# Performance work log

Measured on AMD Instinct MI355X. Metric: run time of the kernel, lower is better.

The kernel has to match this reference:

```python
import math
import jax, jax.numpy as jnp
import numpy as np
from jax import lax

N = 224
EPS_BN = 1e-5


def _conv(x, w, b):
    y = lax.conv_general_dilated(x, w, (1, 1), 'SAME',
                                 dimension_numbers=('NCHW', 'OIHW', 'NCHW'))
    return y + b[None, :, None, None]


def _bn(x, g, beta, m, v):
    # eval-mode BatchNorm2d with running stats
    inv = lax.rsqrt(v + EPS_BN)
    return (x - m[None, :, None, None]) * (g * inv)[None, :, None, None] + beta[None, :, None, None]


def _maxpool2(x):
    return lax.reduce_window(x, -jnp.inf, lax.max, (1, 1, 2, 2), (1, 1, 2, 2), 'VALID')


def setup_inputs() -> dict:
    key = jax.random.key(0)
    ks = jax.random.split(key, 12)
    idx = np.arange(N, dtype=np.float32)
    angles = 2.0 * math.pi * idx[None, :] * idx[:, None] / N
    inp = {
        'sequences': jax.random.normal(ks[0], (16, 8, 3, N, N), dtype=jnp.float32),
        'dft_cos': jnp.asarray(np.cos(angles), dtype=jnp.float32),
        'dft_sin': jnp.asarray(np.sin(angles), dtype=jnp.float32),
        'conv1_w': jax.random.normal(ks[1], (16, 3, 3, 3), dtype=jnp.float32) * 0.1,
        'conv1_b': jnp.zeros((16,), jnp.float32),
        'bn1_g': jnp.ones((16,), jnp.float32),
        'bn1_b': jnp.zeros((16,), jnp.float32),
        'bn1_m': jnp.zeros((16,), jnp.float32),
        'bn1_v': jnp.ones((16,), jnp.float32),
        'conv2_w': jax.random.normal(ks[2], (32, 16, 3, 3), dtype=jnp.float32) * 0.05,
        'conv2_b': jnp.zeros((32,), jnp.float32),
        'bn2_g': jnp.ones((32,), jnp.float32),
        'bn2_b': jnp.zeros((32,), jnp.float32),
        'bn2_m': jnp.zeros((32,), jnp.float32),
        'bn2_v': jnp.ones((32,), jnp.float32),
        'conv3_w': jax.random.normal(ks[3], (64, 32, 3, 3), dtype=jnp.float32) * 0.05,
        'conv3_b': jnp.zeros((64,), jnp.float32),
        'bn3_g': jnp.ones((64,), jnp.float32),
        'bn3_b': jnp.zeros((64,), jnp.float32),
        'bn3_m': jnp.zeros((64,), jnp.float32),
        'bn3_v': jnp.ones((64,), jnp.float32),
        'fc_w': jax.random.normal(ks[4], (128, 64), dtype=jnp.float32) * 0.1,
        'fc_b': jnp.zeros((128,), jnp.float32),
    }
    return inp


def reference(sequences, dft_cos, dft_sin,
              conv1_w, conv1_b, bn1_g, bn1_b, bn1_m, bn1_v,
              conv2_w, conv2_b, bn2_g, bn2_b, bn2_m, bn2_v,
              conv3_w, conv3_b, bn3_g, bn3_b, bn3_m, bn3_v,
              fc_w, fc_b):
    b, s = sequences.shape[0], sequences.shape[1]
    x = sequences[:, s // 2]  # center frames [B,3,H,W]

    # 2D DFT via dense matmul chain: X = (C - jS) x (C - jS)
    C, S = dft_cos, dft_sin
    Cx = jnp.einsum('ij,bcjk->bcik', C, x)
    Sx = jnp.einsum('ij,bcjk->bcik', S, x)
    X_real = jnp.einsum('bcij,jk->bcik', Cx, C) - jnp.einsum('bcij,jk->bcik', Sx, S)
    X_imag = -(jnp.einsum('bcij,jk->bcik', Cx, S) + jnp.einsum('bcij,jk->bcik', Sx, C))
    magnitude = jnp.sqrt(X_real ** 2 + X_imag ** 2 + 1e-08)
    spec = jnp.log(magnitude + 1e-08)
    half = N // 2
    spec = jnp.roll(spec, shift=(half, half), axis=(-2, -1))  # fftshift

    # CNN stack (eval-mode BN, dropout disabled)
    h = jax.nn.relu(_bn(_conv(spec, conv1_w, conv1_b), bn1_g, bn1_b, bn1_m, bn1_v))
    h = _maxpool2(h)
    h = jax.nn.relu(_bn(_conv(h, conv2_w, conv2_b), bn2_g, bn2_b, bn2_m, bn2_v))
    h = _maxpool2(h)
    h = jax.nn.relu(_bn(_conv(h, conv3_w, conv3_b), bn3_g, bn3_b, bn3_m, bn3_v))
    h = jnp.mean(h, axis=(2, 3))  # AdaptiveAvgPool2d((1,1)) + flatten -> [B,64]

    freq_out = jax.nn.relu(h @ fc_w.T + fc_b)  # dropout = identity in eval
    return freq_out
```

## Files before the change

### kernel.cpp

```cpp
#include <hip/hip_runtime.h>
#include <math.h>
#include <stddef.h>

#define N224 224
#define PIX 50176
#define ROWS113 25312

#define OFF_SX    1214976
#define OFF_SPEC  4816896
#define OFF_WT    3211264
#define OFF_WT2   (OFF_WT + 24576)
#define OFF_WT1   (OFF_WT + 30720)
#define OFF_SU3   (OFF_WT + 31296)
#define OFF_SU2   (OFF_WT + 31424)
#define OFF_SU1   (OFF_WT + 31488)
#define OFF_PART  (OFF_WT + 32768)

__global__ __launch_bounds__(256) void prep(
    const float* __restrict__ c1w, const float* __restrict__ c2w,
    const float* __restrict__ c3w, const float* __restrict__ c1b,
    const float* __restrict__ c2b, const float* __restrict__ c3b,
    const float* __restrict__ g1, const float* __restrict__ be1,
    const float* __restrict__ m1, const float* __restrict__ v1,
    const float* __restrict__ g2, const float* __restrict__ be2,
    const float* __restrict__ m2, const float* __restrict__ v2,
    const float* __restrict__ g3, const float* __restrict__ be3,
    const float* __restrict__ m3, const float* __restrict__ v3,
    float* __restrict__ wt3, float* __restrict__ wt2, float* __restrict__ wt1,
    float* __restrict__ su3, float* __restrict__ su2, float* __restrict__ su1)
{
  const int idx = blockIdx.x * 256 + threadIdx.x;
  const int stride = gridDim.x * 256;
  for (int i = idx; i < 32*64*12; i += stride) {
    const int cc = i / 768, r = i % 768, co = r / 12, k = r % 12;
    wt3[i] = (k < 9) ? c3w[co*288 + cc*9 + k] : 0.f;
  }
  for (int i = idx; i < 16*32*12; i += stride) {
    const int cc = i / 384, r = i % 384, co = r / 12, k = r % 12;
    wt2[i] = (k < 9) ? c2w[co*144 + cc*9 + k] : 0.f;
  }
  for (int i = idx; i < 3*16*12; i += stride) {
    const int cc = i / 192, r = i % 192, co = r / 12, k = r % 12;
    wt1[i] = (k < 9) ? c1w[co*27 + cc*9 + k] : 0.f;
  }
  if (idx < 64) {
    const float s = g3[idx] * rsqrtf(v3[idx] + 1e-5f);
    su3[idx] = s; su3[64+idx] = (c3b[idx] - m3[idx]) * s + be3[idx];
  } else if (idx < 96) {
    const int c = idx - 64;
    const float s = g2[c] * rsqrtf(v2[c] + 1e-5f);
    su2[c] = s; su2[32+c] = (c2b[c] - m2[c]) * s + be2[c];
  } else if (idx < 112) {
    const int c = idx - 96;
    const float s = g1[c] * rsqrtf(v1[c] + 1e-5f);
    su1[c] = s; su1[16+c] = (c1b[c] - m1[c]) * s + be1[c];
  }
}

__global__ __launch_bounds__(256) void dft1(
    const float* __restrict__ seq, const float* __restrict__ Cm,
    const float* __restrict__ Sm, float* __restrict__ Cx, float* __restrict__ Sx)
{
  const int p = blockIdx.z;
  const int b = p / 3, ch = p % 3;
  const float* __restrict__ x = seq + ((((size_t)b * 8 + 4) * 3 + ch) * PIX);
  const int i0 = blockIdx.y * 32;
  const int k0 = blockIdx.x * 32;
  const int tid = threadIdx.x;
  const int tx = tid & 15, ty = tid >> 4;
  __shared__ float Ctt[16][36], Stt[16][36], Xt[16][36];
  float aC[2][2] = {{0,0},{0,0}}, aS[2][2] = {{0,0},{0,0}};

  const int sidx = tid & 127;
  const int srow = sidx >> 2;
  const int skq  = (sidx & 3) * 4;
  const bool isC = tid < 128;
  const float* __restrict__ csb = (isC ? Cm : Sm) + (size_t)(i0 + srow) * N224 + skq;
  const int xjr = tid >> 4;
  const int xc  = (tid & 15) * 2;
  const float* __restrict__ xb = x + (size_t)xjr * N224 + k0 + xc;

  for (int jt = 0; jt < 14; ++jt) {
    const int j = jt * 16;
    __syncthreads();
    {
      const float4 v = *(const float4*)(csb + j);
      float (*dst)[36] = isC ? Ctt : Stt;
      dst[skq+0][srow] = v.x; dst[skq+1][srow] = v.y;
      dst[skq+2][srow] = v.z; dst[skq+3][srow] = v.w;
      *(float2*)&Xt[xjr][xc] = *(const float2*)(xb + (size_t)j * N224);
    }
    __syncthreads();
#pragma unroll
    for (int jj = 0; jj < 16; ++jj) {
      const float2 cv = *(const float2*)&Ctt[jj][2*ty];
      const float2 sv = *(const float2*)&Stt[jj][2*ty];
      const float2 xv = *(const float2*)&Xt[jj][2*tx];
      aC[0][0] = fmaf(cv.x, xv.x, aC[0][0]); aC[0][1] = fmaf(cv.x, xv.y, aC[0][1]);
      aC[1][0] = fmaf(cv.y, xv.x, aC[1][0]); aC[1][1] = fmaf(cv.y, xv.y, aC[1][1]);
      aS[0][0] = fmaf(sv.x, xv.x, aS[0][0]); aS[0][1] = fmaf(sv.x, xv.y, aS[0][1]);
      aS[1][0] = fmaf(sv.y, xv.x, aS[1][0]); aS[1][1] = fmaf(sv.y, xv.y, aS[1][1]);
    }
  }
  const size_t b113 = (size_t)p * ROWS113;
#pragma unroll
  for (int a = 0; a < 2; ++a) {
    const int i = i0 + 2*ty + a;
    if (i <= 112) {
      const size_t off = b113 + (size_t)i * N224 + k0 + 2*tx;
      *(float2*)&Cx[off] = make_float2(aC[a][0], aC[a][1]);
      *(float2*)&Sx[off] = make_float2(aS[a][0], aS[a][1]);
    }
  }
}

__global__ __launch_bounds__(256) void dft2(
    const float* __restrict__ Cx, const float* __restrict__ Sx,
    const float* __restrict__ Cm, const float* __restrict__ Sm,
    float* __restrict__ spec)
{
  const int p = blockIdx.z;
  const int i0 = blockIdx.y * 32;
  const int k0 = blockIdx.x * 32;
  const int tid = threadIdx.x;
  const int tx = tid & 15, ty = tid >> 4;
  const size_t b113 = (size_t)p * ROWS113;
  __shared__ float CxT[16][36], SxT[16][36], Ct[16][36], St[16][36];
  float p1[2][2] = {{0,0},{0,0}}, p2[2][2] = {{0,0},{0,0}};
  float p3[2][2] = {{0,0},{0,0}}, p4[2][2] = {{0,0},{0,0}};

  const int sidx = tid & 127;
  const int srow = sidx >> 2;
  const int skq  = (sidx & 3) * 4;
  const bool isCx = tid < 128;
  const int ri = (i0 + srow > 112) ? 112 : i0 + srow;
  const float* __restrict__ ab = (isCx ? Cx : Sx) + b113 + (size_t)ri * N224 + skq;
  const int jr = tid >> 4;
  const int cc2 = (tid & 15) * 2;
  const float* __restrict__ cb = Cm + (size_t)jr * N224 + k0 + cc2;
  const float* __restrict__ sb2 = Sm + (size_t)jr * N224 + k0 + cc2;

  for (int jt = 0; jt < 14; ++jt) {
    const int j = jt * 16;
    __syncthreads();
    {
      const float4 v = *(const float4*)(ab + j);
      float (*dst)[36] = isCx ? CxT : SxT;
      dst[skq+0][srow] = v.x; dst[skq+1][srow] = v.y;
      dst[skq+2][srow] = v.z; dst[skq+3][srow] = v.w;
      *(float2*)&Ct[jr][cc2] = *(const float2*)(cb + (size_t)j * N224);
      *(float2*)&St[jr][cc2] = *(const float2*)(sb2 + (size_t)j * N224);
    }
    __syncthreads();
#pragma unroll
    for (int jj = 0; jj < 16; ++jj) {
      const float2 cxv = *(const float2*)&CxT[jj][2*ty];
      const float2 sxv = *(const float2*)&SxT[jj][2*ty];
      const float2 ccv = *(const float2*)&Ct[jj][2*tx];
      const float2 ssv = *(const float2*)&St[jj][2*tx];
      const float cxa[2] = {cxv.x, cxv.y};
      const float sxa[2] = {sxv.x, sxv.y};
      const float cca[2] = {ccv.x, ccv.y};
      const float ssa[2] = {ssv.x, ssv.y};
#pragma unroll
      for (int a = 0; a < 2; ++a)
#pragma unroll
        for (int d = 0; d < 2; ++d) {
          p1[a][d] = fmaf(cxa[a], cca[d], p1[a][d]);
          p2[a][d] = fmaf(sxa[a], ssa[d], p2[a][d]);
          p3[a][d] = fmaf(cxa[a], ssa[d], p3[a][d]);
          p4[a][d] = fmaf(sxa[a], cca[d], p4[a][d]);
        }
    }
  }
  const size_t sb = (size_t)p * PIX;
#pragma unroll
  for (int a = 0; a < 2; ++a) {
    const int i = i0 + 2*ty + a;
    if (i > 112) continue;
    const int shi  = (i < 112) ? i + 112 : i - 112;
    const int shmi = 112 - i;
    const bool irm = (i >= 1) && (i <= 111);
#pragma unroll
    for (int d = 0; d < 2; ++d) {
      const int k = k0 + 2*tx + d;
      if (k > 112) continue;
      const float r1 = p1[a][d] - p2[a][d];
      const float i1 = p3[a][d] + p4[a][d];
      const float sp1v = logf(sqrtf(fmaf(r1, r1, fmaf(i1, i1, 1e-8f))) + 1e-8f);
      const float r2v = p1[a][d] + p2[a][d];
      const float i2v = p3[a][d] - p4[a][d];
      const float sp2v = logf(sqrtf(fmaf(r2v, r2v, fmaf(i2v, i2v, 1e-8f))) + 1e-8f);
      const int shk  = (k < 112) ? k + 112 : k - 112;
      const int shmk = 112 - k;
      const bool krm = (k >= 1) && (k <= 111);
      spec[sb + (size_t)shi*N224 + shk] = sp1v;
      if (irm)        spec[sb + (size_t)shmi*N224 + shk ] = sp2v;
      if (krm)        spec[sb + (size_t)shi *N224 + shmk] = sp2v;
      if (irm && krm) spec[sb + (size_t)shmi*N224 + shmk] = sp1v;
    }
  }
}

__global__ __launch_bounds__(256) void conv1(
    const float* __restrict__ spec, const float* __restrict__ wt1,
    const float* __restrict__ su1, float* __restrict__ out)
{
  const int band = blockIdx.x, b = blockIdx.y;
  const int tid = threadIdx.x;
  const int lane = tid & 63, w = tid >> 6;
  const int co = lane & 15, cr = (lane >> 4) & 1, xs = lane >> 5;
  const int xh = w >> 1, xq = w & 1;
  __shared__ float in_t[3][4][232];
  for (int i = tid; i < 3*4*232; i += 256) {
    const int c = i % 232, r = (i / 232) % 4, cc = i / 928;
    const int y = band*2 - 1 + r, gx = c - 1;
    float v = 0.f;
    if (c < 226 && y >= 0 && y < 224 && gx >= 0 && gx < 224)
      v = spec[((size_t)b*3 + cc) * PIX + (size_t)y * N224 + gx];
    in_t[cc][r][c] = v;
  }
  __syncthreads();
  const int X0 = xh*112 + xq*56 + xs*28;
  float acc[28];
#pragma unroll
  for (int px = 0; px < 28; ++px) acc[px] = 0.f;
#pragma unroll
  for (int cc = 0; cc < 3; ++cc) {
    const float4 w0 = *(const float4*)&wt1[cc*192 + co*12];
    const float4 w1 = *(const float4*)&wt1[cc*192 + co*12 + 4];
    const float  w8 = wt1[cc*192 + co*12 + 8];
    const float wr[9] = {w0.x, w0.y, w0.z, w0.w, w1.x, w1.y, w1.z, w1.w, w8};
#pragma unroll
    for (int ky = 0; ky < 3; ++ky) {
      float xr[32];
      const float4* rp = (const float4*)&in_t[cc][cr + ky][X0];
#pragma unroll
      for (int t = 0; t < 8; ++t) {
        const float4 v = rp[t];
        xr[4*t]=v.x; xr[4*t+1]=v.y; xr[4*t+2]=v.z; xr[4*t+3]=v.w;
      }
#pragma unroll
      for (int px = 0; px < 28; ++px) {
        acc[px] = fmaf(xr[px  ], wr[ky*3  ], acc[px]);
        acc[px] = fmaf(xr[px+1], wr[ky*3+1], acc[px]);
        acc[px] = fmaf(xr[px+2], wr[ky*3+2], acc[px]);
      }
    }
  }
  const float s = su1[co], u = su1[16+co];
  float m[14];
#pragma unroll
  for (int p = 0; p < 14; ++p)
    m[p] = fmaxf(acc[2*p]*s + u, acc[2*p+1]*s + u);
#pragma unroll
  for (int p = 0; p < 14; ++p) {
    const float pm = __shfl_xor(m[p], 16);
    m[p] = fmaxf(fmaxf(m[p], pm), 0.f);
  }
  if (cr == 0) {
    const int pxb = X0 >> 1;
    float* op = &out[(((size_t)b*16 + co)*112 + band)*112 + pxb];
#pragma unroll
    for (int p = 0; p < 14; ++p) op[p] = m[p];
  }
}

__global__ __launch_bounds__(256) void conv2(
    const float* __restrict__ h1, const float* __restrict__ wt2,
    const float* __restrict__ su2, float* __restrict__ out)
{
  const int xh = blockIdx.x, band = blockIdx.y, b = blockIdx.z;
  const int tid = threadIdx.x;
  const int lane = tid & 63, w = tid >> 6;
  const int co = lane & 31, cr = lane >> 5;
  __shared__ float in_t[16][4][64];
  for (int i = tid; i < 16*4*58; i += 256) {
    const int c = i % 58, r = (i / 58) % 4, cc = i / 232;
    const int y = band*2 - 1 + r, gx = xh*56 - 1 + c;
    float v = 0.f;
    if (y >= 0 && y < 112 && gx >= 0 && gx < 112)
      v = h1[(((size_t)b*16 + cc)*112 + y)*112 + gx];
    in_t[cc][r][c] = v;
  }
  __syncthreads();
  const int X0 = w * 14;
  float acc[14];
#pragma unroll
  for (int px = 0; px < 14; ++px) acc[px] = 0.f;
  const float* __restrict__ wp = wt2 + co*12;
  float4 nw0 = *(const float4*)(wp);
  float4 nw1 = *(const float4*)(wp + 4);
  float  nw8 = wp[8];
  for (int cc = 0; cc < 16; ++cc) {
    const float4 w0 = nw0, w1 = nw1; const float w8 = nw8;
    if (cc < 15) {
      const float* np = wp + (cc + 1) * 384;
      nw0 = *(const float4*)(np);
      nw1 = *(const float4*)(np + 4);
      nw8 = np[8];
    }
    const float wr[9] = {w0.x, w0.y, w0.z, w0.w, w1.x, w1.y, w1.z, w1.w, w8};
    float xr[3][16];
#pragma unroll
    for (int ky = 0; ky < 3; ++ky) {
      const float2* rp = (const float2*)&in_t[cc][cr + ky][X0];
#pragma unroll
      for (int t = 0; t < 8; ++t) {
        const float2 v = rp[t];
        xr[ky][2*t] = v.x; xr[ky][2*t+1] = v.y;
      }
    }
#pragma unroll
    for (int ky = 0; ky < 3; ++ky)
#pragma unroll
      for (int px = 0; px < 14; ++px) {
        acc[px] = fmaf(xr[ky][px  ], wr[ky*3  ], acc[px]);
        acc[px] = fmaf(xr[ky][px+1], wr[ky*3+1], acc[px]);
        acc[px] = fmaf(xr[ky][px+2], wr[ky*3+2], acc[px]);
      }
  }
  const float s = su2[co], u = su2[32+co];
  float m[7];
#pragma unroll
  for (int p = 0; p < 7; ++p)
    m[p] = fmaxf(acc[2*p]*s + u, acc[2*p+1]*s + u);
#pragma unroll
  for (int p = 0; p < 7; ++p) {
    const float pm = __shfl_xor(m[p], 32);
    m[p] = fmaxf(fmaxf(m[p], pm), 0.f);
  }
  if (cr == 0) {
    float* op = &out[(((size_t)b*32 + co)*56 + band)*56 + xh*28 + w*7];
#pragma unroll
    for (int p = 0; p < 7; ++p) op[p] = m[p];
  }
}

__global__ __launch_bounds__(256) void conv3(
    const float* __restrict__ h2, const float* __restrict__ wt3,
    const float* __restrict__ su3, float* __restrict__ part)
{
  const int band = blockIdx.x, b = blockIdx.y;
  const int tid = threadIdx.x;
  const int co = tid & 63, w = tid >> 6;
  __shared__ float in_t[32][3][64];
  __shared__ float red[4][64];
  for (int i = tid; i < 32*3*58; i += 256) {
    const int c = i % 58, r = (i / 58) % 3, cc = i / 174;
    const int y = band - 1 + r, gx = c - 1;
    float v = 0.f;
    if (y >= 0 && y < 56 && gx >= 0 && gx < 56)
      v = h2[(((size_t)b*32 + cc)*56 + y)*56 + gx];
    in_t[cc][r][c] = v;
  }
  __syncthreads();
  const int X0 = w * 14;
  float acc[14];
#pragma unroll
  for (int px = 0; px < 14; ++px) acc[px] = 0.f;
  const float* __restrict__ wp = wt3 + co*12;
  float4 nw0 = *(const float4*)(wp);
  float4 nw1 = *(const float4*)(wp + 4);
  float  nw8 = wp[8];
  for (int cc = 0; cc < 32; ++cc) {
    const float4 w0 = nw0, w1 = nw1; const float w8 = nw8;
    if (cc < 31) {
      const float* np = wp + (cc + 1) * 768;
      nw0 = *(const float4*)(np);
      nw1 = *(const float4*)(np + 4);
      nw8 = np[8];
    }
    const float wr[9] = {w0.x, w0.y, w0.z, w0.w, w1.x, w1.y, w1.z, w1.w, w8};
    float xr[3][16];
#pragma unroll
    for (int rr = 0; rr < 3; ++rr) {
      const float2* rp = (const float2*)&in_t[cc][rr][X0];
#pragma unroll
      for (int t = 0; t < 8; ++t) {
        const float2 v = rp[t];
        xr[rr][2*t] = v.x; xr[rr][2*t+1] = v.y;
      }
    }
#pragma unroll
    for (int rr = 0; rr < 3; ++rr)
#pragma unroll
      for (int px = 0; px < 14; ++px) {
        acc[px] = fmaf(xr[rr][px  ], wr[rr*3  ], acc[px]);
        acc[px] = fmaf(xr[rr][px+1], wr[rr*3+1], acc[px]);
        acc[px] = fmaf(xr[rr][px+2], wr[rr*3+2], acc[px]);
      }
  }
  const float s = su3[co], u = su3[64+co];
  float sum = 0.f;
#pragma unroll
  for (int px = 0; px < 14; ++px)
    sum += fmaxf(acc[px]*s + u, 0.f);
  red[w][co] = sum;
  __syncthreads();
  if (tid < 64)
    part[((size_t)b*64 + co)*56 + band] =
        red[0][co] + red[1][co] + red[2][co] + red[3][co];
}

__global__ __launch_bounds__(128) void mean_fc(
    const float* __restrict__ part, const float* __restrict__ fw,
    const float* __restrict__ fb, float* __restrict__ out)
{
  const int b = blockIdx.x;
  const int tid = threadIdx.x;
  __shared__ float h3s[64];
  if (tid < 64) {
    float s = 0.f;
    const float* pp = part + ((size_t)b*64 + tid)*56;
#pragma unroll
    for (int i = 0; i < 56; ++i) s += pp[i];
    h3s[tid] = s * (1.0f / 3136.0f);
  }
  __syncthreads();
  float acc = fb[tid];
#pragma unroll
  for (int c = 0; c < 64; ++c)
    acc = fmaf(h3s[c], fw[tid*64 + c], acc);
  out[b*128 + tid] = fmaxf(acc, 0.f);
}

extern "C" void kernel_launch(void* const* d_in, const int* in_sizes, int n_in,
                              void* d_out, int out_size, void* d_ws, size_t ws_size,
                              hipStream_t stream) {
  const float* seq  = (const float*)d_in[0];
  const float* dcos = (const float*)d_in[1];
  const float* dsin = (const float*)d_in[2];
  const float* c1w  = (const float*)d_in[3];
  const float* c1b  = (const float*)d_in[4];
  const float* b1g  = (const float*)d_in[5];
  const float* b1b  = (const float*)d_in[6];
  const float* b1m  = (const float*)d_in[7];
  const float* b1v  = (const float*)d_in[8];
  const float* c2w  = (const float*)d_in[9];
  const float* c2b  = (const float*)d_in[10];
  const float* b2g  = (const float*)d_in[11];
  const float* b2b  = (const float*)d_in[12];
  const float* b2m  = (const float*)d_in[13];
  const float* b2v  = (const float*)d_in[14];
  const float* c3w  = (const float*)d_in[15];
  const float* c3b  = (const float*)d_in[16];
  const float* b3g  = (const float*)d_in[17];
  const float* b3b  = (const float*)d_in[18];
  const float* b3m  = (const float*)d_in[19];
  const float* b3v  = (const float*)d_in[20];
  const float* fw   = (const float*)d_in[21];
  const float* fb   = (const float*)d_in[22];
  float* out = (float*)d_out;

  float* ws   = (float*)d_ws;
  float* Cx   = ws;
  float* Sx   = ws + OFF_SX;
  float* spec = ws + OFF_SPEC;
  float* h1   = ws;
  float* h2   = ws + OFF_SPEC;
  float* wt3  = ws + OFF_WT;
  float* wt2  = ws + OFF_WT2;
  float* wt1  = ws + OFF_WT1;
  float* su3  = ws + OFF_SU3;
  float* su2  = ws + OFF_SU2;
  float* su1  = ws + OFF_SU1;
  float* part = ws + OFF_PART;

  prep<<<24, 256, 0, stream>>>(c1w, c2w, c3w, c1b, c2b, c3b,
                               b1g, b1b, b1m, b1v, b2g, b2b, b2m, b2v,
                               b3g, b3b, b3m, b3v, wt3, wt2, wt1, su3, su2, su1);
  dft1<<<dim3(7, 4, 48), 256, 0, stream>>>(seq, dcos, dsin, Cx, Sx);
  dft2<<<dim3(4, 4, 48), 256, 0, stream>>>(Cx, Sx, dcos, dsin, spec);
  conv1<<<dim3(112, 16), 256, 0, stream>>>(spec, wt1, su1, h1);
  conv2<<<dim3(2, 56, 16), 256, 0, stream>>>(h1, wt2, su2, h2);
  conv3<<<dim3(56, 16), 256, 0, stream>>>(h2, wt3, su3, part);
  mean_fc<<<16, 128, 0, stream>>>(part, fw, fb, out);
}
```

Measured before the change: 164.1 us.

## Register-block conv3 over two output channels with half-width pixel strips

```diff
diff --git a/kernel.cpp b/kernel.cpp
--- a/kernel.cpp
+++ b/kernel.cpp
@@ -337,14 +337,15 @@
   }
 }
 
-__global__ __launch_bounds__(256) void conv3(
+__global__ __launch_bounds__(256, 2) void conv3(
     const float* __restrict__ h2, const float* __restrict__ wt3,
     const float* __restrict__ su3, float* __restrict__ part)
 {
   const int band = blockIdx.x, b = blockIdx.y;
   const int tid = threadIdx.x;
-  const int co = tid & 63, w = tid >> 6;
-  __shared__ float in_t[32][3][64];
+  const int lane = tid & 63, w = tid >> 6;
+  const int co = lane & 31, xs = lane >> 5;
+  __shared__ float in_t[32][3][60];
   __shared__ float red[4][64];
   for (int i = tid; i < 32*3*58; i += 256) {
     const int c = i % 58, r = (i / 58) % 3, cc = i / 174;
@@ -355,52 +356,65 @@
     in_t[cc][r][c] = v;
   }
   __syncthreads();
-  const int X0 = w * 14;
-  float acc[14];
-#pragma unroll
-  for (int px = 0; px < 14; ++px) acc[px] = 0.f;
-  const float* __restrict__ wp = wt3 + co*12;
-  float4 nw0 = *(const float4*)(wp);
-  float4 nw1 = *(const float4*)(wp + 4);
-  float  nw8 = wp[8];
+  const int X0 = (w*2 + xs) * 7;
+  float accA[7], accB[7];
+#pragma unroll
+  for (int px = 0; px < 7; ++px) { accA[px] = 0.f; accB[px] = 0.f; }
+  const float* __restrict__ wpA = wt3 + co*12;
+  const float* __restrict__ wpB = wt3 + (co + 32)*12;
+  float4 nA0 = *(const float4*)(wpA);
+  float4 nA1 = *(const float4*)(wpA + 4);
+  float  nA8 = wpA[8];
+  float4 nB0 = *(const float4*)(wpB);
+  float4 nB1 = *(const float4*)(wpB + 4);
+  float  nB8 = wpB[8];
   for (int cc = 0; cc < 32; ++cc) {
-    const float4 w0 = nw0, w1 = nw1; const float w8 = nw8;
+    const float4 a0 = nA0, a1 = nA1; const float a8 = nA8;
+    const float4 b0 = nB0, b1 = nB1; const float b8 = nB8;
     if (cc < 31) {
-      const float* np = wp + (cc + 1) * 768;
-      nw0 = *(const float4*)(np);
-      nw1 = *(const float4*)(np + 4);
-      nw8 = np[8];
-    }
-    const float wr[9] = {w0.x, w0.y, w0.z, w0.w, w1.x, w1.y, w1.z, w1.w, w8};
-    float xr[3][16];
-#pragma unroll
-    for (int rr = 0; rr < 3; ++rr) {
-      const float2* rp = (const float2*)&in_t[cc][rr][X0];
-#pragma unroll
-      for (int t = 0; t < 8; ++t) {
-        const float2 v = rp[t];
-        xr[rr][2*t] = v.x; xr[rr][2*t+1] = v.y;
+      const float* npA = wpA + (cc + 1) * 768;
+      const float* npB = wpB + (cc + 1) * 768;
+      nA0 = *(const float4*)(npA); nA1 = *(const float4*)(npA + 4); nA8 = npA[8];
+      nB0 = *(const float4*)(npB); nB1 = *(const float4*)(npB + 4); nB8 = npB[8];
+    }
+    const float wA[9] = {a0.x, a0.y, a0.z, a0.w, a1.x, a1.y, a1.z, a1.w, a8};
+    const float wB[9] = {b0.x, b0.y, b0.z, b0.w, b1.x, b1.y, b1.z, b1.w, b8};
+    float xv[3][10];
+#pragma unroll
+    for (int rr = 0; rr < 3; ++rr)
+#pragma unroll
+      for (int j = 0; j < 10; ++j)
+        xv[rr][j] = in_t[cc][rr][X0 + j];
+#pragma unroll
+    for (int rr = 0; rr < 3; ++rr)
+#pragma unroll
+      for (int px = 0; px < 7; ++px) {
+        accA[px] = fmaf(xv[rr][px  ], wA[rr*3  ], accA[px]);
+        accA[px] = fmaf(xv[rr][px+1], wA[rr*3+1], accA[px]);
+        accA[px] = fmaf(xv[rr][px+2], wA[rr*3+2], accA[px]);
+        accB[px] = fmaf(xv[rr][px  ], wB[rr*3  ], accB[px]);
+        accB[px] = fmaf(xv[rr][px+1], wB[rr*3+1], accB[px]);
+        accB[px] = fmaf(xv[rr][px+2], wB[rr*3+2], accB[px]);
       }
-    }
-#pragma unroll
-    for (int rr = 0; rr < 3; ++rr)
-#pragma unroll
-      for (int px = 0; px < 14; ++px) {
-        acc[px] = fmaf(xr[rr][px  ], wr[rr*3  ], acc[px]);
-        acc[px] = fmaf(xr[rr][px+1], wr[rr*3+1], acc[px]);
-        acc[px] = fmaf(xr[rr][px+2], wr[rr*3+2], acc[px]);
-      }
-  }
-  const float s = su3[co], u = su3[64+co];
-  float sum = 0.f;
-#pragma unroll
-  for (int px = 0; px < 14; ++px)
-    sum += fmaxf(acc[px]*s + u, 0.f);
-  red[w][co] = sum;
+  }
+  const float sA = su3[co],    uA = su3[64+co];
+  const float sB = su3[co+32], uB = su3[96+co];
+  float sumA = 0.f, sumB = 0.f;
+#pragma unroll
+  for (int px = 0; px < 7; ++px) {
+    sumA += fmaxf(accA[px]*sA + uA, 0.f);
+    sumB += fmaxf(accB[px]*sB + uB, 0.f);
+  }
+  sumA += __shfl_xor(sumA, 32);
+  sumB += __shfl_xor(sumB, 32);
+  if (xs == 0) {
+    red[w][co]      = sumA;
+    red[w][co + 32] = sumB;
+  }
   __syncthreads();
   if (tid < 64)
-    part[((size_t)b*64 + co)*56 + band] =
-        red[0][co] + red[1][co] + red[2][co] + red[3][co];
+    part[((size_t)b*64 + tid)*56 + band] =
+        red[0][tid] + red[1][tid] + red[2][tid] + red[3][tid];
 }
 
 __global__ __launch_bounds__(128) void mean_fc(
```

Measured after the change: 166.7 us. Within noise of the previous version (+1.6%).

## Split conv3 input channels across blocks with separate reduction kernel

Applied to the files above, without the earlier changes.

```diff
diff --git a/kernel.cpp b/kernel.cpp
--- a/kernel.cpp
+++ b/kernel.cpp
@@ -341,31 +341,31 @@
     const float* __restrict__ h2, const float* __restrict__ wt3,
     const float* __restrict__ su3, float* __restrict__ part)
 {
-  const int band = blockIdx.x, b = blockIdx.y;
+  const int ccq = blockIdx.x, band = blockIdx.y, b = blockIdx.z;
   const int tid = threadIdx.x;
   const int co = tid & 63, w = tid >> 6;
-  __shared__ float in_t[32][3][64];
+  __shared__ float in_t[8][3][64];
   __shared__ float red[4][64];
-  for (int i = tid; i < 32*3*58; i += 256) {
-    const int c = i % 58, r = (i / 58) % 3, cc = i / 174;
+  for (int i = tid; i < 8*3*58; i += 256) {
+    const int c = i % 58, r = (i / 58) % 3, ccl = i / 174;
     const int y = band - 1 + r, gx = c - 1;
     float v = 0.f;
     if (y >= 0 && y < 56 && gx >= 0 && gx < 56)
-      v = h2[(((size_t)b*32 + cc)*56 + y)*56 + gx];
-    in_t[cc][r][c] = v;
+      v = h2[(((size_t)b*32 + ccq*8 + ccl)*56 + y)*56 + gx];
+    in_t[ccl][r][c] = v;
   }
   __syncthreads();
   const int X0 = w * 14;
   float acc[14];
 #pragma unroll
   for (int px = 0; px < 14; ++px) acc[px] = 0.f;
-  const float* __restrict__ wp = wt3 + co*12;
+  const float* __restrict__ wp = wt3 + (size_t)ccq*8*768 + co*12;
   float4 nw0 = *(const float4*)(wp);
   float4 nw1 = *(const float4*)(wp + 4);
   float  nw8 = wp[8];
-  for (int cc = 0; cc < 32; ++cc) {
+  for (int cc = 0; cc < 8; ++cc) {
     const float4 w0 = nw0, w1 = nw1; const float w8 = nw8;
-    if (cc < 31) {
+    if (cc < 7) {
       const float* np = wp + (cc + 1) * 768;
       nw0 = *(const float4*)(np);
       nw1 = *(const float4*)(np + 4);
@@ -391,20 +391,41 @@
         acc[px] = fmaf(xr[rr][px+2], wr[rr*3+2], acc[px]);
       }
   }
+  {
+  }
+  const size_t base = ((((size_t)b*56 + band)*64 + co)*4 + ccq)*56 + X0;
+#pragma unroll
+  for (int px = 0; px < 14; ++px)
+    part[base + px] = acc[px];
+}
+
+__global__ __launch_bounds__(256) void conv3_fin(
+    const float* __restrict__ part, const float* __restrict__ su3,
+    float* __restrict__ rowsum)
+{
+  const int band = blockIdx.x, b = blockIdx.y;
+  const int tid = threadIdx.x;
+  const int co = tid & 63, w = tid >> 6;
+  __shared__ float red[4][64];
+  const int X0 = w * 14;
+  const size_t base = (((size_t)b*56 + band)*64 + co)*4*56;
   const float s = su3[co], u = su3[64+co];
   float sum = 0.f;
 #pragma unroll
-  for (int px = 0; px < 14; ++px)
-    sum += fmaxf(acc[px]*s + u, 0.f);
+  for (int px = 0; px < 14; ++px) {
+    const float v = part[base + X0 + px] + part[base + 56 + X0 + px]
+                  + part[base + 112 + X0 + px] + part[base + 168 + X0 + px];
+    sum += fmaxf(v*s + u, 0.f);
+  }
   red[w][co] = sum;
   __syncthreads();
   if (tid < 64)
-    part[((size_t)b*64 + co)*56 + band] =
-        red[0][co] + red[1][co] + red[2][co] + red[3][co];
+    rowsum[((size_t)b*64 + tid)*56 + band] =
+        red[0][tid] + red[1][tid] + red[2][tid] + red[3][tid];
 }
 
 __global__ __launch_bounds__(128) void mean_fc(
-    const float* __restrict__ part, const float* __restrict__ fw,
+    const float* __restrict__ rowsum, const float* __restrict__ fw,
     const float* __restrict__ fb, float* __restrict__ out)
 {
   const int b = blockIdx.x;
@@ -412,7 +433,7 @@
   __shared__ float h3s[64];
   if (tid < 64) {
     float s = 0.f;
-    const float* pp = part + ((size_t)b*64 + tid)*56;
+    const float* pp = rowsum + ((size_t)b*64 + tid)*56;
 #pragma unroll
     for (int i = 0; i < 56; ++i) s += pp[i];
     h3s[tid] = s * (1.0f / 3136.0f);
@@ -466,6 +487,9 @@
   float* su2  = ws + OFF_SU2;
   float* su1  = ws + OFF_SU1;
   float* part = ws + OFF_PART;
+  part = ws;
+  float* partpx = ws + 6422528;
+  float* rowsum = ws + OFF_PART;
 
   prep<<<24, 256, 0, stream>>>(c1w, c2w, c3w, c1b, c2b, c3b,
                                b1g, b1b, b1m, b1v, b2g, b2b, b2m, b2v,
@@ -474,6 +498,7 @@
   dft2<<<dim3(4, 4, 48), 256, 0, stream>>>(Cx, Sx, dcos, dsin, spec);
   conv1<<<dim3(112, 16), 256, 0, stream>>>(spec, wt1, su1, h1);
   conv2<<<dim3(2, 56, 16), 256, 0, stream>>>(h1, wt2, su2, h2);
-  conv3<<<dim3(56, 16), 256, 0, stream>>>(h2, wt3, su3, part);
-  mean_fc<<<16, 128, 0, stream>>>(part, fw, fb, out);
-}
+  conv3<<<dim3(4, 56, 16), 256, 0, stream>>>(h2, wt3, su3, partpx);
+  conv3_fin<<<dim3(56, 16), 256, 0, stream>>>(partpx, su3, rowsum);
+  mean_fc<<<16, 128, 0, stream>>>(rowsum, fw, fb, out);
+}
```

Result: slower. 176.4 us (+7.5%).
